# Performance work log

Hardware: AMD Instinct MI355X
Metric: run time of the kernel (lower is better)

Reference implementation:

```python
import jax, jax.numpy as jnp
import numpy as np

N_HEADS = 16
ROPE_BASE = 10000.0


def _rope_tables(T, head_dim, dtype):
    inv_freq = 1.0 / (ROPE_BASE ** (jnp.arange(0, head_dim, 2, dtype=jnp.float32) / head_dim))
    t = jnp.arange(T, dtype=jnp.float32)
    freqs = jnp.outer(t, inv_freq)              # (T, head_dim/2)
    emb = jnp.concatenate([freqs, freqs], -1)   # (T, head_dim)
    return jnp.cos(emb).astype(dtype), jnp.sin(emb).astype(dtype)


def _rotate_half(x):
    x1, x2 = jnp.split(x, 2, axis=-1)
    return jnp.concatenate([-x2, x1], axis=-1)


def setup_inputs() -> dict:
    key = jax.random.key(0)
    k1, k2, k3 = jax.random.split(key, 3)
    B, T, C = 2, 2048, 2048
    x = jax.random.normal(k1, (B, T, C), dtype=jnp.float32)
    Wqkv = jax.random.normal(k2, (C, 3 * C), dtype=jnp.float32) * (1.0 / np.sqrt(C))
    Wproj = jax.random.normal(k3, (C, C), dtype=jnp.float32) * (1.0 / np.sqrt(C))
    return {"x": x, "Wqkv": Wqkv, "Wproj": Wproj}


def reference(x, Wqkv, Wproj):
    B, T, C = x.shape
    H = N_HEADS
    D = C // H
    qkv = jnp.einsum('btc,cd->btd', x, Wqkv)            # (B,T,3C)
    q, k, v = jnp.split(qkv, 3, axis=-1)
    # (B,T,C) -> (B,H,T,D)
    q = q.reshape(B, T, H, D).transpose(0, 2, 1, 3)
    k = k.reshape(B, T, H, D).transpose(0, 2, 1, 3)
    v = v.reshape(B, T, H, D).transpose(0, 2, 1, 3)
    cos, sin = _rope_tables(T, D, x.dtype)              # (T,D) each
    q = q * cos + _rotate_half(q) * sin
    k = k * cos + _rotate_half(k) * sin
    scale = 1.0 / jnp.sqrt(jnp.asarray(D, x.dtype))
    att = jnp.einsum('bhqd,bhkd->bhqk', q, k) * scale   # (B,H,T,T)
    causal = jnp.tril(jnp.ones((T, T), dtype=bool))
    att = jnp.where(causal, att, jnp.asarray(-jnp.inf, att.dtype))
    att = jax.nn.softmax(att, axis=-1)
    y = jnp.einsum('bhqk,bhkd->bhqd', att, v)           # (B,H,T,D)
    y = y.transpose(0, 2, 1, 3).reshape(B, T, C)
    return jnp.einsum('btc,cd->btd', y, Wproj)
```

## Files before the change

kernel.cpp:

```cpp
#include <hip/hip_runtime.h>
#include <stdint.h>

#define T_SEQ 2048
#define NH 16
#define HD 128
#define CC 2048
#define N3 6144
#define MM 4096

typedef short bf16x8 __attribute__((ext_vector_type(8)));
typedef float f32x4 __attribute__((ext_vector_type(4)));
typedef float f32x16 __attribute__((ext_vector_type(16)));
typedef unsigned int u32x4 __attribute__((ext_vector_type(4)));

__device__ __forceinline__ unsigned short f2bf(float f) {
  unsigned int u = __float_as_uint(f);
  u += 0x7FFF + ((u >> 16) & 1);
  return (unsigned short)(u >> 16);
}
__device__ __forceinline__ float bf2f(unsigned short h) {
  return __uint_as_float(((unsigned int)h) << 16);
}
__device__ __forceinline__ unsigned int cvt_pk_bf16(float lo, float hi) {
  unsigned int r;
  asm("v_cvt_pk_bf16_f32 %0, %1, %2" : "=v"(r) : "v"(lo), "v"(hi));
  return r;
}

__global__ __launch_bounds__(256) void k_transpose_cvt(const float* __restrict__ in,
                                                       unsigned short* __restrict__ out,
                                                       int K, int N) {
  __shared__ float tile[32][33];
  int k0 = blockIdx.x * 32;
  int n0 = blockIdx.y * 32;
  int tx = threadIdx.x & 31, ty = threadIdx.x >> 5;
  #pragma unroll
  for (int r = ty; r < 32; r += 8)
    tile[r][tx] = in[(size_t)(k0 + r) * N + n0 + tx];
  __syncthreads();
  #pragma unroll
  for (int r = ty; r < 32; r += 8)
    out[(size_t)(n0 + r) * K + k0 + tx] = f2bf(tile[tx][r]);
}

__global__ __launch_bounds__(256) void k_cvt(const float* __restrict__ in,
                                             unsigned short* __restrict__ out, int n4) {
  int i = blockIdx.x * 256 + threadIdx.x;
  if (i >= n4) return;
  float4 v = ((const float4*)in)[i];
  ushort4 o;
  o.x = f2bf(v.x); o.y = f2bf(v.y); o.z = f2bf(v.z); o.w = f2bf(v.w);
  ((ushort4*)out)[i] = o;
}

template<int NJ, int EPI, int MMAJ>
__global__ __launch_bounds__(512, 1) void k_gemm8(const unsigned short* __restrict__ A,
                                                  const unsigned short* __restrict__ Bt,
                                                  float* __restrict__ C,
                                                  unsigned short* __restrict__ qo,
                                                  unsigned short* __restrict__ ko,
                                                  unsigned short* __restrict__ vo,
                                                  int M, int N, int K) {
  constexpr int BU = NJ / 2;
  constexpr int DSTRIDE = (1 + BU) * 16384;
  extern __shared__ __align__(16) char lds[];
  const int tid = threadIdx.x;
  const int lane = tid & 63;
  const int lr = lane & 15, lg = lane >> 4;
  const int wave = tid >> 6;
  const int wm = wave >> 2, wn = wave & 3;
  const int nwg = gridDim.x;
  const int bid = blockIdx.x;
  const int wg = (bid & 7) * (nwg >> 3) + (bid >> 3);
  const int GX = M >> 7;
  const int GN = N / (NJ * 64);
  const int mt = MMAJ ? (wg % GX) : (wg / GN);
  const int nt = MMAJ ? (wg / GX) : (wg % GN);
  const int m0 = mt * 128, n0 = nt * NJ * 64;
  const int NT = K >> 6;

  auto STAGE = [&](int d, int op, int h, int t) {
    const unsigned short* src = op ? Bt : A;
    const int r0 = (op ? n0 + h * 128 : m0);
    const int kc = t * 64;
    char* base = lds + d * DSTRIDE + op * 16384 + h * 16384;
    #pragma unroll
    for (int l = 0; l < 2; ++l) {
      int p = (l * 512 + tid) * 16;
      int qq = p ^ (((p >> 7) & 7) << 4);
      const unsigned short* g = src + (size_t)(r0 + (qq >> 7)) * K + kc + ((qq & 127) >> 1);
      __builtin_amdgcn_global_load_lds(
          (const __attribute__((address_space(1))) void*)g,
          (__attribute__((address_space(3))) void*)(base + (l * 512 + (tid & 448)) * 16),
          16, 0, 0);
    }
  };
  auto RD = [&](int d, int op, int row, int kb) -> bf16x8 {
    const char* base = lds + d * DSTRIDE + op * 16384;
    int p = row * 128 + kb;
    p ^= ((p >> 7) & 7) << 4;
    return *(const bf16x8*)(base + p);
  };

  f32x4 acc[4][NJ];
  #pragma unroll
  for (int i = 0; i < 4; ++i)
    #pragma unroll
    for (int j = 0; j < NJ; ++j) acc[i][j] = (f32x4){0.f, 0.f, 0.f, 0.f};

  bf16x8 bfrg[NJ][2];

#define PHASE(D, MI, READB, DOST, SD, SO, SH, ST, VM)                                    \
  {                                                                                      \
    if (READB) {                                                                         \
      _Pragma("unroll")                                                                  \
      for (int nj = 0; nj < NJ; ++nj)                                                    \
        _Pragma("unroll")                                                                \
        for (int ks = 0; ks < 2; ++ks)                                                   \
          bfrg[nj][ks] = RD(D, 1, wn * NJ * 16 + nj * 16 + lr, ks * 64 + lg * 16);       \
    }                                                                                    \
    bf16x8 af[2];                                                                        \
    _Pragma("unroll")                                                                    \
    for (int ks = 0; ks < 2; ++ks)                                                       \
      af[ks] = RD(D, 0, wm * 64 + (MI) * 16 + lr, ks * 64 + lg * 16);                    \
    if (DOST) STAGE(SD, SO, SH, ST);                                                     \
    __builtin_amdgcn_s_barrier();                                                        \
    asm volatile("s_waitcnt lgkmcnt(0)" ::: "memory");                                   \
    __builtin_amdgcn_s_setprio(1);                                                       \
    _Pragma("unroll")                                                                    \
    for (int nj = 0; nj < NJ; ++nj)                                                      \
      _Pragma("unroll")                                                                  \
      for (int ks = 0; ks < 2; ++ks)                                                     \
        acc[MI][nj] = __builtin_amdgcn_mfma_f32_16x16x32_bf16(af[ks], bfrg[nj][ks], acc[MI][nj], 0, 0, 0); \
    __builtin_amdgcn_s_setprio(0);                                                       \
    if ((VM) == 6) asm volatile("s_waitcnt vmcnt(6)" ::: "memory");                      \
    if ((VM) == 4) asm volatile("s_waitcnt vmcnt(4)" ::: "memory");                      \
    __builtin_amdgcn_s_barrier();                                                        \
  }

  const int t1 = NT > 1 ? 1 : 0;
  #pragma unroll
  for (int h = 0; h < BU; ++h) STAGE(0, 1, h, 0);
  STAGE(0, 0, 0, 0);
  #pragma unroll
  for (int h = 0; h < BU; ++h) STAGE(1, 1, h, t1);
  if (NJ == 6) asm volatile("s_waitcnt vmcnt(6)" ::: "memory");
  else         asm volatile("s_waitcnt vmcnt(4)" ::: "memory");
  __builtin_amdgcn_s_barrier();

  for (int it = 0; it < (NT >> 1); ++it) {
    const int tb  = 2 * it + 1;
    const int ta1 = min(2 * it + 2, NT - 1);
    const int tb1 = min(2 * it + 3, NT - 1);
    if (NJ == 6) {
      PHASE(0, 0, true,  true, 1, 0, 0, tb,  -1)
      PHASE(0, 1, false, true, 0, 1, 0, ta1, -1)
      PHASE(0, 2, false, true, 0, 1, 1, ta1, -1)
      PHASE(0, 3, false, true, 0, 1, 2, ta1,  6)
      PHASE(1, 0, true,  true, 0, 0, 0, ta1, -1)
      PHASE(1, 1, false, true, 1, 1, 0, tb1, -1)
      PHASE(1, 2, false, true, 1, 1, 1, tb1, -1)
      PHASE(1, 3, false, true, 1, 1, 2, tb1,  6)
    } else {
      PHASE(0, 0, true,  true,  1, 0, 0, tb,  -1)
      PHASE(0, 1, false, true,  0, 1, 0, ta1, -1)
      PHASE(0, 2, false, true,  0, 1, 1, ta1, -1)
      PHASE(0, 3, false, false, 0, 0, 0, 0,    4)
      PHASE(1, 0, true,  true,  0, 0, 0, ta1, -1)
      PHASE(1, 1, false, true,  1, 1, 0, tb1, -1)
      PHASE(1, 2, false, true,  1, 1, 1, tb1, -1)
      PHASE(1, 3, false, false, 0, 0, 0, 0,    4)
    }
  }
#undef PHASE

  #pragma unroll
  for (int mi = 0; mi < 4; ++mi) {
    #pragma unroll
    for (int nj = 0; nj < NJ; ++nj) {
      #pragma unroll
      for (int j = 0; j < 4; ++j) {
        int m = m0 + wm * 64 + mi * 16 + lg * 4 + j;
        int n = n0 + wn * NJ * 16 + nj * 16 + lr;
        float val = acc[mi][nj][j];
        if (EPI == 0) {
          C[(size_t)m * N + n] = val;
        } else {
          int which = n >> 11, cc = n & 2047;
          int h = cc >> 7, d = cc & 127;
          int b = m >> 11, t = m & 2047;
          unsigned short* dst = which == 0 ? qo : (which == 1 ? ko : vo);
          dst[(((size_t)(b * NH + h)) * T_SEQ + t) * HD + d] = f2bf(val);
        }
      }
    }
  }
}

__global__ __launch_bounds__(256) void k_rope(unsigned short* __restrict__ q,
                                              unsigned short* __restrict__ k) {
  int i = blockIdx.x * 256 + threadIdx.x;
  int d = i & 63;
  int t = (i >> 6) & (T_SEQ - 1);
  int bh = i >> 17;
  float invf = exp2f((float)(-2 * d) * (13.287712379549449f / 128.f));
  float ang = (float)t * invf;
  float c = cosf(ang), s = sinf(ang);
  size_t base = ((size_t)bh * T_SEQ + t) * HD + d;
  const float scale = 0.12751741562076117f;
  float q1 = bf2f(q[base]), q2 = bf2f(q[base + 64]);
  q[base]      = f2bf((q1 * c - q2 * s) * scale);
  q[base + 64] = f2bf((q2 * c + q1 * s) * scale);
  float k1 = bf2f(k[base]), k2 = bf2f(k[base + 64]);
  k[base]      = f2bf(k1 * c - k2 * s);
  k[base + 64] = f2bf(k2 * c + k1 * s);
}

__global__ __launch_bounds__(256) void k_transpose_v(const unsigned short* __restrict__ in,
                                                     unsigned short* __restrict__ out) {
  __shared__ unsigned short tile[32][33];
  int bh = blockIdx.z;
  int t0 = blockIdx.x * 32, d0 = blockIdx.y * 32;
  int tx = threadIdx.x & 31, ty = threadIdx.x >> 5;
  const unsigned short* src = in + (size_t)bh * T_SEQ * HD;
  unsigned short* dst = out + (size_t)bh * HD * T_SEQ;
  #pragma unroll
  for (int r = ty; r < 32; r += 8)
    tile[r][tx] = src[(size_t)(t0 + r) * HD + d0 + tx];
  __syncthreads();
  #pragma unroll
  for (int r = ty; r < 32; r += 8)
    dst[(size_t)(d0 + r) * T_SEQ + t0 + tx] = tile[tx][r];
}

__global__ __launch_bounds__(256, 2) void k_attn(const unsigned short* __restrict__ Q,
                                                 const unsigned short* __restrict__ K,
                                                 const unsigned short* __restrict__ Vt,
                                                 unsigned short* __restrict__ Y) {
  __shared__ __align__(16) unsigned short Kls[2][64 * 128];
  __shared__ __align__(16) unsigned short Vls[2][128 * 64];
  const int id = blockIdx.x;
  const int sub = id & 255;
  const int bh = sub & 31;
  const int qtl = (id < 256) ? (15 - (sub >> 5)) : (sub >> 5);
  const int b = bh >> 4, h = bh & 15;
  const int tid = threadIdx.x, wv = tid >> 6, lane = tid & 63;
  const int l31 = lane & 31, hh = lane >> 5;
  const int q0 = qtl * 128;
  const int jtmax = 2 * qtl + 1;
  const int qglob = q0 + wv * 32 + l31;
  const unsigned short* Qb = Q + (size_t)bh * T_SEQ * HD;
  const unsigned short* Kb = K + (size_t)bh * T_SEQ * HD;
  const unsigned short* Vb = Vt + (size_t)bh * HD * T_SEQ;

  auto STAGEKV = [&](int tk, int bb) {
    #pragma unroll
    for (int ch = 0; ch < 4; ++ch) {
      int p = (ch * 256 + tid) * 16;
      int q = p ^ (((p >> 8) & 7) << 4);
      const unsigned short* g = Kb + (size_t)(tk + (q >> 8)) * HD + ((q & 255) >> 1);
      __builtin_amdgcn_global_load_lds(
          (const __attribute__((address_space(1))) void*)g,
          (__attribute__((address_space(3))) void*)((char*)Kls[bb] + (ch * 256 + (tid & 192)) * 16),
          16, 0, 0);
    }
    #pragma unroll
    for (int ch = 0; ch < 4; ++ch) {
      int p = (ch * 256 + tid) * 16;
      int q = p ^ (((p >> 7) & 7) << 4);
      const unsigned short* g = Vb + (size_t)(q >> 7) * T_SEQ + tk + ((q & 127) >> 1);
      __builtin_amdgcn_global_load_lds(
          (const __attribute__((address_space(1))) void*)g,
          (__attribute__((address_space(3))) void*)((char*)Vls[bb] + (ch * 256 + (tid & 192)) * 16),
          16, 0, 0);
    }
  };

  bf16x8 qfr[8];
  #pragma unroll
  for (int c = 0; c < 8; ++c)
    qfr[c] = *(const bf16x8*)(Qb + (size_t)qglob * HD + c * 16 + hh * 8);

  f32x16 oacc[4];
  #pragma unroll
  for (int dt = 0; dt < 4; ++dt)
    #pragma unroll
    for (int r = 0; r < 16; ++r) oacc[dt][r] = 0.f;
  float mrun = -1e30f, lrun = 0.f;

  STAGEKV(0, 0);
  asm volatile("s_waitcnt vmcnt(0)" ::: "memory");
  __syncthreads();

  for (int jt = 0; jt <= jtmax; ++jt) {
    const int cur = jt & 1;
    if (jt < jtmax) STAGEKV((jt + 1) * 64, cur ^ 1);

    f32x16 sacc[2];
    #pragma unroll
    for (int t = 0; t < 2; ++t)
      #pragma unroll
      for (int r = 0; r < 16; ++r) sacc[t][r] = 0.f;
    __builtin_amdgcn_s_setprio(1);
    #pragma unroll
    for (int s = 0; s < 8; ++s) {
      #pragma unroll
      for (int t = 0; t < 2; ++t) {
        int row = t * 32 + l31;
        int byte = (row * 256 + s * 32 + hh * 16) ^ ((row & 7) << 4);
        bf16x8 kf = *(const bf16x8*)((const char*)Kls[cur] + byte);
        sacc[t] = __builtin_amdgcn_mfma_f32_32x32x16_bf16(kf, qfr[s], sacc[t], 0, 0, 0);
      }
    }
    __builtin_amdgcn_s_setprio(0);

    if (jt >= 2 * qtl) {
      #pragma unroll
      for (int t = 0; t < 2; ++t)
        #pragma unroll
        for (int r = 0; r < 16; ++r) {
          int kg = jt * 64 + t * 32 + (r & 3) + 8 * (r >> 2) + 4 * hh;
          if (kg > qglob) sacc[t][r] = -1e30f;
        }
    }

    float pmax = sacc[0][0];
    #pragma unroll
    for (int r = 1; r < 16; ++r) pmax = fmaxf(pmax, sacc[0][r]);
    #pragma unroll
    for (int r = 0; r < 16; ++r) pmax = fmaxf(pmax, sacc[1][r]);
    pmax = fmaxf(pmax, __shfl_xor(pmax, 32));

    if (__any(pmax > mrun + 8.0f)) {
      float mnew = fmaxf(mrun, pmax);
      float osc = exp2f(mrun - mnew);
      lrun *= osc;
      mrun = mnew;
      #pragma unroll
      for (int r = 0; r < 16; ++r) {
        int qr = (r & 3) + 8 * (r >> 2) + 4 * hh;
        float sr = __shfl(osc, qr);
        #pragma unroll
        for (int dt = 0; dt < 4; ++dt) oacc[dt][r] *= sr;
      }
    }

    unsigned int pk[16];
    float rsum = 0.f;
    #pragma unroll
    for (int t = 0; t < 2; ++t)
      #pragma unroll
      for (int i = 0; i < 8; ++i) {
        float p0 = exp2f(sacc[t][2 * i] - mrun);
        float p1 = exp2f(sacc[t][2 * i + 1] - mrun);
        rsum += p0 + p1;
        pk[t * 8 + i] = cvt_pk_bf16(p0, p1);
      }
    rsum += __shfl_xor(rsum, 32);
    lrun += rsum;

    bf16x8 pa[4];
    #pragma unroll
    for (int c = 0; c < 4; ++c) {
      int base = (c >> 1) * 8 + (c & 1) * 4;
      unsigned int s0 = hh == 0 ? pk[base + 2] : pk[base + 0];
      unsigned int s1 = hh == 0 ? pk[base + 3] : pk[base + 1];
      unsigned int r0 = __shfl_xor((int)s0, 32);
      unsigned int r1 = __shfl_xor((int)s1, 32);
      u32x4 f;
      f[0] = hh == 0 ? pk[base + 0] : r0;
      f[1] = hh == 0 ? pk[base + 1] : r1;
      f[2] = hh == 0 ? r0 : pk[base + 2];
      f[3] = hh == 0 ? r1 : pk[base + 3];
      pa[c] = *(bf16x8*)&f;
    }

    __builtin_amdgcn_s_setprio(1);
    #pragma unroll
    for (int dt = 0; dt < 4; ++dt) {
      #pragma unroll
      for (int c = 0; c < 4; ++c) {
        int row = dt * 32 + l31;
        int byte = (row * 128 + c * 32 + hh * 16) ^ ((row & 7) << 4);
        bf16x8 vf = *(const bf16x8*)((const char*)Vls[cur] + byte);
        oacc[dt] = __builtin_amdgcn_mfma_f32_32x32x16_bf16(pa[c], vf, oacc[dt], 0, 0, 0);
      }
    }
    __builtin_amdgcn_s_setprio(0);

    asm volatile("s_waitcnt vmcnt(0)" ::: "memory");
    __syncthreads();
  }

  float linv = 1.0f / lrun;
  #pragma unroll
  for (int r = 0; r < 16; ++r) {
    int qr = (r & 3) + 8 * (r >> 2) + 4 * hh;
    float li = __shfl(linv, qr);
    int qg = q0 + wv * 32 + qr;
    size_t base = ((size_t)b * T_SEQ + qg) * CC + h * HD;
    #pragma unroll
    for (int dt = 0; dt < 4; ++dt)
      Y[base + dt * 32 + l31] = f2bf(oacc[dt][r] * li);
  }
}

extern "C" void kernel_launch(void* const* d_in, const int* in_sizes, int n_in,
                              void* d_out, int out_size, void* d_ws, size_t ws_size,
                              hipStream_t stream) {
  const float* x     = (const float*)d_in[0];
  const float* Wqkv  = (const float*)d_in[1];
  const float* Wproj = (const float*)d_in[2];
  float* out = (float*)d_out;
  char* ws = (char*)d_ws;
  const size_t MB = 1024 * 1024;
  unsigned short* WqkvT  = (unsigned short*)(ws + 0);
  unsigned short* vt     = (unsigned short*)(ws + 0);
  unsigned short* WprojT = (unsigned short*)(ws + 24 * MB);
  unsigned short* xb     = (unsigned short*)(ws + 32 * MB);
  unsigned short* y      = xb;
  unsigned short* q      = (unsigned short*)(ws + 48 * MB);
  unsigned short* k      = (unsigned short*)(ws + 64 * MB);
  unsigned short* v      = (unsigned short*)(ws + 80 * MB);

  k_transpose_cvt<<<dim3(CC / 32, N3 / 32), 256, 0, stream>>>(Wqkv, WqkvT, CC, N3);
  k_transpose_cvt<<<dim3(CC / 32, CC / 32), 256, 0, stream>>>(Wproj, WprojT, CC, CC);
  k_cvt<<<(MM * CC / 4) / 256, 256, 0, stream>>>(x, xb, MM * CC / 4);
  k_gemm8<6, 1, 1><<<dim3((MM / 128) * (N3 / 384)), 512, 131072, stream>>>(
      xb, WqkvT, nullptr, q, k, v, MM, N3, CC);
  k_rope<<<(32 * T_SEQ * 64) / 256, 256, 0, stream>>>(q, k);
  k_transpose_v<<<dim3(T_SEQ / 32, HD / 32, 32), 256, 0, stream>>>(v, vt);
  k_attn<<<dim3(512), 256, 0, stream>>>(q, k, vt, y);
  k_gemm8<4, 0, 0><<<dim3((MM / 128) * (CC / 256)), 512, 98304, stream>>>(
      y, WprojT, out, nullptr, nullptr, nullptr, MM, CC, CC);
}
```

Baseline: 271.1 us.

## Software-pipeline PV matmul with next QK and fuse Q RoPE into attention

```diff
diff --git a/kernel.cpp b/kernel.cpp
--- a/kernel.cpp
+++ b/kernel.cpp
@@ -197,8 +197,7 @@
   }
 }
 
-__global__ __launch_bounds__(256) void k_rope(unsigned short* __restrict__ q,
-                                              unsigned short* __restrict__ k) {
+__global__ __launch_bounds__(256) void k_ropek(unsigned short* __restrict__ k) {
   int i = blockIdx.x * 256 + threadIdx.x;
   int d = i & 63;
   int t = (i >> 6) & (T_SEQ - 1);
@@ -207,10 +206,6 @@
   float ang = (float)t * invf;
   float c = cosf(ang), s = sinf(ang);
   size_t base = ((size_t)bh * T_SEQ + t) * HD + d;
-  const float scale = 0.12751741562076117f;
-  float q1 = bf2f(q[base]), q2 = bf2f(q[base + 64]);
-  q[base]      = f2bf((q1 * c - q2 * s) * scale);
-  q[base + 64] = f2bf((q2 * c + q1 * s) * scale);
   float k1 = bf2f(k[base]), k2 = bf2f(k[base + 64]);
   k[base]      = f2bf(k1 * c - k2 * s);
   k[base + 64] = f2bf(k2 * c + k1 * s);
@@ -237,8 +232,9 @@
                                                  const unsigned short* __restrict__ K,
                                                  const unsigned short* __restrict__ Vt,
                                                  unsigned short* __restrict__ Y) {
-  __shared__ __align__(16) unsigned short Kls[2][64 * 128];
-  __shared__ __align__(16) unsigned short Vls[2][128 * 64];
+  extern __shared__ __align__(16) char alds[];
+  char* Kls = alds;
+  char* Vls = alds + 32768;
   const int id = blockIdx.x;
   const int sub = id & 255;
   const int bh = sub & 31;
@@ -253,7 +249,8 @@
   const unsigned short* Kb = K + (size_t)bh * T_SEQ * HD;
   const unsigned short* Vb = Vt + (size_t)bh * HD * T_SEQ;
 
-  auto STAGEKV = [&](int tk, int bb) {
+  auto STAGEK = [&](int tk, int s) {
+    char* base = Kls + s * 16384;
     #pragma unroll
     for (int ch = 0; ch < 4; ++ch) {
       int p = (ch * 256 + tid) * 16;
@@ -261,9 +258,12 @@
       const unsigned short* g = Kb + (size_t)(tk + (q >> 8)) * HD + ((q & 255) >> 1);
       __builtin_amdgcn_global_load_lds(
           (const __attribute__((address_space(1))) void*)g,
-          (__attribute__((address_space(3))) void*)((char*)Kls[bb] + (ch * 256 + (tid & 192)) * 16),
+          (__attribute__((address_space(3))) void*)(base + (ch * 256 + (tid & 192)) * 16),
           16, 0, 0);
     }
+  };
+  auto STAGEV = [&](int tk, int s) {
+    char* base = Vls + s * 16384;
     #pragma unroll
     for (int ch = 0; ch < 4; ++ch) {
       int p = (ch * 256 + tid) * 16;
@@ -271,7 +271,7 @@
       const unsigned short* g = Vb + (size_t)(q >> 7) * T_SEQ + tk + ((q & 127) >> 1);
       __builtin_amdgcn_global_load_lds(
           (const __attribute__((address_space(1))) void*)g,
-          (__attribute__((address_space(3))) void*)((char*)Vls[bb] + (ch * 256 + (tid & 192)) * 16),
+          (__attribute__((address_space(3))) void*)(base + (ch * 256 + (tid & 192)) * 16),
           16, 0, 0);
     }
   };
@@ -280,6 +280,23 @@
   #pragma unroll
   for (int c = 0; c < 8; ++c)
     qfr[c] = *(const bf16x8*)(Qb + (size_t)qglob * HD + c * 16 + hh * 8);
+  {
+    const float SCALE = 0.12751741562076117f;
+    const float L2I = 13.287712379549449f / 64.f;
+    #pragma unroll
+    for (int c = 0; c < 4; ++c) {
+      #pragma unroll
+      for (int e = 0; e < 8; ++e) {
+        int d = c * 16 + hh * 8 + e;
+        float ang = (float)qglob * exp2f(-(float)d * L2I);
+        float cs = cosf(ang), sn = sinf(ang);
+        float lo = bf2f((unsigned short)qfr[c][e]);
+        float hi = bf2f((unsigned short)qfr[c + 4][e]);
+        qfr[c][e]     = (short)f2bf((lo * cs - hi * sn) * SCALE);
+        qfr[c + 4][e] = (short)f2bf((hi * cs + lo * sn) * SCALE);
+      }
+    }
+  }
 
   f32x16 oacc[4];
   #pragma unroll
@@ -287,32 +304,55 @@
     #pragma unroll
     for (int r = 0; r < 16; ++r) oacc[dt][r] = 0.f;
   float mrun = -1e30f, lrun = 0.f;
-
-  STAGEKV(0, 0);
+  bf16x8 paP[4];
+
+  STAGEK(0, 0); STAGEV(0, 0);
   asm volatile("s_waitcnt vmcnt(0)" ::: "memory");
   __syncthreads();
 
+  auto PV = [&](const bf16x8* pa, int vs) {
+    const char* base = Vls + vs * 16384;
+    __builtin_amdgcn_s_setprio(1);
+    #pragma unroll
+    for (int dt = 0; dt < 4; ++dt) {
+      #pragma unroll
+      for (int c = 0; c < 4; ++c) {
+        int row = dt * 32 + l31;
+        int byte = (row * 128 + c * 32 + hh * 16) ^ ((row & 7) << 4);
+        bf16x8 vf = *(const bf16x8*)(base + byte);
+        oacc[dt] = __builtin_amdgcn_mfma_f32_32x32x16_bf16(pa[c], vf, oacc[dt], 0, 0, 0);
+      }
+    }
+    __builtin_amdgcn_s_setprio(0);
+  };
+
+  int vcur = 0;
   for (int jt = 0; jt <= jtmax; ++jt) {
-    const int cur = jt & 1;
-    if (jt < jtmax) STAGEKV((jt + 1) * 64, cur ^ 1);
+    const int kcur = jt & 1;
+    const int vnext = (vcur == 2) ? 0 : vcur + 1;
+    const int vprev = (vcur == 0) ? 2 : vcur - 1;
+    if (jt < jtmax) { STAGEK((jt + 1) * 64, kcur ^ 1); STAGEV((jt + 1) * 64, vnext); }
 
     f32x16 sacc[2];
     #pragma unroll
     for (int t = 0; t < 2; ++t)
       #pragma unroll
       for (int r = 0; r < 16; ++r) sacc[t][r] = 0.f;
-    __builtin_amdgcn_s_setprio(1);
-    #pragma unroll
-    for (int s = 0; s < 8; ++s) {
-      #pragma unroll
-      for (int t = 0; t < 2; ++t) {
-        int row = t * 32 + l31;
-        int byte = (row * 256 + s * 32 + hh * 16) ^ ((row & 7) << 4);
-        bf16x8 kf = *(const bf16x8*)((const char*)Kls[cur] + byte);
-        sacc[t] = __builtin_amdgcn_mfma_f32_32x32x16_bf16(kf, qfr[s], sacc[t], 0, 0, 0);
-      }
-    }
-    __builtin_amdgcn_s_setprio(0);
+    {
+      const char* kbase = Kls + kcur * 16384;
+      __builtin_amdgcn_s_setprio(1);
+      #pragma unroll
+      for (int s = 0; s < 8; ++s) {
+        #pragma unroll
+        for (int t = 0; t < 2; ++t) {
+          int row = t * 32 + l31;
+          int byte = (row * 256 + s * 32 + hh * 16) ^ ((row & 7) << 4);
+          bf16x8 kf = *(const bf16x8*)(kbase + byte);
+          sacc[t] = __builtin_amdgcn_mfma_f32_32x32x16_bf16(kf, qfr[s], sacc[t], 0, 0, 0);
+        }
+      }
+      __builtin_amdgcn_s_setprio(0);
+    }
 
     if (jt >= 2 * qtl) {
       #pragma unroll
@@ -324,6 +364,8 @@
         }
     }
 
+    if (jt > 0) PV(paP, vprev);
+
     float pmax = sacc[0][0];
     #pragma unroll
     for (int r = 1; r < 16; ++r) pmax = fmaxf(pmax, sacc[0][r]);
@@ -359,7 +401,6 @@
     rsum += __shfl_xor(rsum, 32);
     lrun += rsum;
 
-    bf16x8 pa[4];
     #pragma unroll
     for (int c = 0; c < 4; ++c) {
       int base = (c >> 1) * 8 + (c & 1) * 4;
@@ -372,25 +413,16 @@
       f[1] = hh == 0 ? pk[base + 1] : r1;
       f[2] = hh == 0 ? r0 : pk[base + 2];
       f[3] = hh == 0 ? r1 : pk[base + 3];
-      pa[c] = *(bf16x8*)&f;
-    }
-
-    __builtin_amdgcn_s_setprio(1);
-    #pragma unroll
-    for (int dt = 0; dt < 4; ++dt) {
-      #pragma unroll
-      for (int c = 0; c < 4; ++c) {
-        int row = dt * 32 + l31;
-        int byte = (row * 128 + c * 32 + hh * 16) ^ ((row & 7) << 4);
-        bf16x8 vf = *(const bf16x8*)((const char*)Vls[cur] + byte);
-        oacc[dt] = __builtin_amdgcn_mfma_f32_32x32x16_bf16(pa[c], vf, oacc[dt], 0, 0, 0);
-      }
-    }
-    __builtin_amdgcn_s_setprio(0);
-
-    asm volatile("s_waitcnt vmcnt(0)" ::: "memory");
+      paP[c] = *(bf16x8*)&f;
+    }
+
+    asm volatile("s_waitcnt vmcnt(8)" ::: "memory");
     __syncthreads();
-  }
+    vcur = vnext;
+  }
+
+  asm volatile("s_waitcnt vmcnt(0)" ::: "memory");
+  PV(paP, jtmax % 3);
 
   float linv = 1.0f / lrun;
   #pragma unroll
@@ -428,9 +460,9 @@
   k_cvt<<<(MM * CC / 4) / 256, 256, 0, stream>>>(x, xb, MM * CC / 4);
   k_gemm8<6, 1, 1><<<dim3((MM / 128) * (N3 / 384)), 512, 131072, stream>>>(
       xb, WqkvT, nullptr, q, k, v, MM, N3, CC);
-  k_rope<<<(32 * T_SEQ * 64) / 256, 256, 0, stream>>>(q, k);
+  k_ropek<<<(32 * T_SEQ * 64) / 256, 256, 0, stream>>>(k);
   k_transpose_v<<<dim3(T_SEQ / 32, HD / 32, 32), 256, 0, stream>>>(v, vt);
-  k_attn<<<dim3(512), 256, 0, stream>>>(q, k, vt, y);
+  k_attn<<<dim3(512), 256, 81920, stream>>>(q, k, vt, y);
   k_gemm8<4, 0, 0><<<dim3((MM / 128) * (CC / 256)), 512, 98304, stream>>>(
       y, WprojT, out, nullptr, nullptr, nullptr, MM, CC, CC);
 }
```

Result: slower. 394.9 us (+45.6%).
